# Kernel tuning notes

Measured on AMD Instinct MI355X. Metric: run time of the kernel, lower is better.

Reference implementation:

```python
import jax, jax.numpy as jnp
import numpy as np

N = 100000      # nodes (patches)
NNZ = 800000    # incidence (node, hyperedge) pairs from H.coo()
E = 16384       # hyperedges
IN = 128        # in_dim == hidden_dim (residual path active)
HID = 128
HEADS = 4
HD = HID // HEADS   # 32, per-head out_dim
QD = 64             # type_query_dim
L = 2               # n_layers
NT = 4              # n_node_types
ET = 3              # n_edge_types


def setup_inputs() -> dict:
    key = jax.random.key(0)
    ks = jax.random.split(key, 12)
    f32 = jnp.float32
    return {
        "x": jax.random.normal(ks[0], (N, IN), f32),
        "node_types": jax.random.randint(ks[1], (N,), 0, NT, jnp.int32),
        "node_idx": jax.random.randint(ks[2], (NNZ,), 0, N, jnp.int32),
        "edge_idx": jax.random.randint(ks[3], (NNZ,), 0, E, jnp.int32),
        "edge_type": jax.random.randint(ks[4], (E,), 0, ET, jnp.int32),
        # per-layer, per-head parameters (leading axes L, HEADS)
        "type_query": (jax.random.normal(ks[5], (L, HEADS, NT, QD), f32) * 0.02),
        "fc1_w": jax.random.normal(ks[6], (L, HEADS, IN + QD, 32), f32) / np.sqrt(IN + QD),
        "fc1_b": jnp.zeros((L, HEADS, 32), f32),
        "fc2_w": jax.random.normal(ks[7], (L, HEADS, 32, 1), f32) / np.sqrt(32.0),
        "fc2_b": jnp.zeros((L, HEADS, 1), f32),
        "Wq": jax.random.normal(ks[8], (L, HEADS, IN, HD), f32) / np.sqrt(IN),
        "Wv": jax.random.normal(ks[9], (L, HEADS, IN, HD), f32) / np.sqrt(IN),
        "edge_ctx": jax.random.normal(ks[10], (L, HEADS, ET, HD), f32) * 0.02,
        "ln_g": jnp.ones((L, HID), f32),
        "ln_b": jnp.zeros((L, HID), f32),
    }


def _seg_softmax(a, seg, num):
    # scatter_softmax over segments `seg` (stable: subtract per-segment max)
    m = jax.ops.segment_max(a, seg, num_segments=num)
    ex = jnp.exp(a - m[seg])
    s = jax.ops.segment_sum(ex, seg, num_segments=num)
    return ex / s[seg]


def _head(h, node_types, node_idx, edge_idx, edge_type, tq, w1, b1, w2, b2, wq, wv, ec):
    # CascadedHyperGAT.forward, one head
    sig = tq[node_types]                                      # (N, QD)
    z = jnp.tanh(jnp.concatenate([h, sig], axis=1) @ w1 + b1)  # (N, 32)
    alpha_type = jax.nn.sigmoid(z @ w2 + b2)[:, 0]             # (N,)
    Q = h @ wq                                                 # (N, HD)
    V = h @ wv                                                 # (N, HD)
    ctx = ec[edge_type][edge_idx]                              # (NNZ, HD)
    a = jnp.sum(Q[node_idx] * ctx, axis=1)                     # (NNZ,)
    a = jnp.where(a >= 0, a, 0.2 * a)                          # leaky_relu(0.2)
    a = a * alpha_type[node_idx]
    attn = _seg_softmax(a, edge_idx, E)                        # (NNZ,)
    edge_feat = jax.ops.segment_sum(attn[:, None] * V[node_idx], edge_idx, num_segments=E)
    node_feat = jax.ops.segment_sum(attn[:, None] * edge_feat[edge_idx], node_idx, num_segments=N)
    return node_feat, edge_feat


def _layernorm(h, g, b, eps=1e-5):
    mu = h.mean(-1, keepdims=True)
    var = ((h - mu) ** 2).mean(-1, keepdims=True)
    return (h - mu) * jax.lax.rsqrt(var + eps) * g + b


def reference(x, node_types, node_idx, edge_idx, edge_type,
              type_query, fc1_w, fc1_b, fc2_w, fc2_b, Wq, Wv, edge_ctx, ln_g, ln_b):
    head_v = jax.vmap(_head, in_axes=(None, None, None, None, None, 0, 0, 0, 0, 0, 0, 0, 0))
    stats = [x]
    h = x
    for l in range(L):  # small static layer count
        nf, _ = head_v(h, node_types, node_idx, edge_idx, edge_type,
                       type_query[l], fc1_w[l], fc1_b[l], fc2_w[l], fc2_b[l],
                       Wq[l], Wv[l], edge_ctx[l])            # (HEADS, N, HD)
        hn = jnp.transpose(nf, (1, 0, 2)).reshape(h.shape[0], -1)  # concat heads -> (N, HID)
        if hn.shape == h.shape:
            hn = hn + h                                       # residual (dims match)
        h = _layernorm(hn, ln_g[l], ln_b[l])
        stats.append(h)
    return jnp.concatenate(stats, axis=-1)                    # (N, IN + HID*L)
```

## Files before the change

kernel.cpp:

```cpp
#include <hip/hip_runtime.h>
#include <math.h>

#define HEADS 4
#define HD 32
#define QD 64
#define DIN 128
#define NTYPES 4
#define ETYPES 3
#define CAP 512
#define WTC 272

typedef __attribute__((ext_vector_type(8))) short bf16x8;
typedef __attribute__((ext_vector_type(4))) float f32x4;
typedef unsigned short ushort_t;

static inline int cdiv(int a, int b){ return (a + b - 1) / b; }

__device__ inline unsigned short f2bf(float f){
  unsigned u = __float_as_uint(f);
  unsigned r = (u + 0x7FFF + ((u >> 16) & 1)) >> 16;
  return (unsigned short)r;
}
__device__ inline float bf2f(unsigned short u){ return __uint_as_float(((unsigned)u) << 16); }

__device__ inline float lgt_get(const ushort_t* __restrict__ lgt, int n, int et, int hh){
  uint2 lg = *(const uint2*)((const char*)lgt + (size_t)n*24 + et*8);
  unsigned u = (hh & 2) ? lg.y : lg.x;
  return bf2f((hh & 1) ? (ushort_t)(u >> 16) : (ushort_t)(u & 0xffff));
}

__device__ inline void accum8(float* ef, uint4 w, float e){
  ef[0] += e*bf2f((ushort_t)(w.x & 0xffff)); ef[1] += e*bf2f((ushort_t)(w.x >> 16));
  ef[2] += e*bf2f((ushort_t)(w.y & 0xffff)); ef[3] += e*bf2f((ushort_t)(w.y >> 16));
  ef[4] += e*bf2f((ushort_t)(w.z & 0xffff)); ef[5] += e*bf2f((ushort_t)(w.z >> 16));
  ef[6] += e*bf2f((ushort_t)(w.w & 0xffff)); ef[7] += e*bf2f((ushort_t)(w.w >> 16));
}


__global__ __launch_bounds__(256) void hist_k(const int* __restrict__ node_idx,
                                              const int* __restrict__ edge_idx,
                                              int* __restrict__ cnt,
                                              uint2* __restrict__ ranks, int E, int NNZ)
{
  int i = blockIdx.x*256 + threadIdx.x;
  if (i < NNZ){
    unsigned re = (unsigned)atomicAdd(&cnt[edge_idx[i]], 1);
    unsigned rn = (unsigned)atomicAdd(&cnt[E + node_idx[i]], 1);
    uint2 r; r.x = re; r.y = rn;
    ranks[i] = r;
  }
}

__global__ __launch_bounds__(1024) void scan_pass1(const int* __restrict__ in, int* __restrict__ bsums, int n)
{
  __shared__ int sd[1024];
  int i = blockIdx.x*1024 + threadIdx.x;
  sd[threadIdx.x] = (i < n) ? in[i] : 0;
  __syncthreads();
  for (int s = 512; s > 0; s >>= 1){
    if (threadIdx.x < s) sd[threadIdx.x] += sd[threadIdx.x + s];
    __syncthreads();
  }
  if (threadIdx.x == 0) bsums[blockIdx.x] = sd[0];
}

__global__ __launch_bounds__(1024) void scan_pass2(int* __restrict__ bsums, int nb)
{
  __shared__ int sd[1024];
  int v = (threadIdx.x < nb) ? bsums[threadIdx.x] : 0;
  sd[threadIdx.x] = v;
  __syncthreads();
  for (int s = 1; s < 1024; s <<= 1){
    int t = (threadIdx.x >= s) ? sd[threadIdx.x - s] : 0;
    __syncthreads();
    sd[threadIdx.x] += t;
    __syncthreads();
  }
  if (threadIdx.x < nb) bsums[threadIdx.x] = sd[threadIdx.x] - v;
}

__global__ __launch_bounds__(1024) void scan_pass3(const int* __restrict__ in, const int* __restrict__ bsums,
                                                   int* __restrict__ out, int n)
{
  __shared__ int sd[1024];
  int i = blockIdx.x*1024 + threadIdx.x;
  int v = (i < n) ? in[i] : 0;
  sd[threadIdx.x] = v;
  __syncthreads();
  for (int s = 1; s < 1024; s <<= 1){
    int t = (threadIdx.x >= s) ? sd[threadIdx.x - s] : 0;
    __syncthreads();
    sd[threadIdx.x] += t;
    __syncthreads();
  }
  if (i < n) out[i] = bsums[blockIdx.x] + sd[threadIdx.x] - v;
}

__global__ __launch_bounds__(256) void scatter_k(const int* __restrict__ node_idx, const int* __restrict__ edge_idx,
                                                 const uint2* __restrict__ ranks,
                                                 const int* __restrict__ off,
                                                 uint2* __restrict__ srtE_rec, int E, int NNZ)
{
  int i = blockIdx.x*256 + threadIdx.x;
  if (i >= NNZ) return;
  int n = node_idx[i], e = edge_idx[i];
  uint2 r = ranks[i];
  int pe = off[e] + (int)r.x;
  int pn = off[E + n] - NNZ + (int)r.y;
  uint2 rec; rec.x = (unsigned)n; rec.y = (unsigned)pn;
  srtE_rec[pe] = rec;
}


__global__ __launch_bounds__(128) void wtprep_k(const float* __restrict__ w1, const float* __restrict__ wv,
                                                short* __restrict__ Wt, int L)
{
  int c = blockIdx.x % 256, l = blockIdx.x / 256;
  int k = threadIdx.x;
  int hh = (c >> 5) & 3, j = c & 31;
  float v;
  if (c < 128) v = w1[((((size_t)l*HEADS + hh)*(DIN+QD)) + k)*32 + j];
  else         v = wv[((((size_t)l*HEADS + hh)*DIN) + k)*32 + j];
  Wt[((size_t)l*WTC + c)*128 + k] = (short)f2bf(v);
}

__global__ __launch_bounds__(128) void wqc_k(const float* __restrict__ wq, const float* __restrict__ ec,
                                             short* __restrict__ Wt)
{
  int b = blockIdx.x;
  int l = b / 12, c = b % 12, h = c / 3, et = c % 3;
  int k = threadIdx.x;
  const float* wrow = wq + ((((size_t)l*HEADS + h)*DIN) + k)*32;
  const float* ecp  = ec + (((size_t)l*HEADS + h)*ETYPES + et)*32;
  float s = 0.f;
  #pragma unroll
  for (int d = 0; d < 32; d++) s += wrow[d] * ecp[d];
  Wt[((size_t)l*WTC + 256 + c)*128 + k] = (short)f2bf(s);
}

__global__ __launch_bounds__(32) void sbias_k(const float* __restrict__ tq, const float* __restrict__ w1,
                                              const float* __restrict__ b1, float* __restrict__ sbias)
{
  int b = blockIdx.x;
  int ty = b % NTYPES; int hh = (b / NTYPES) % HEADS; int l = b / (NTYPES*HEADS);
  int j = threadIdx.x;
  const float* tqp = tq + (((size_t)l*HEADS + hh)*NTYPES + ty)*QD;
  const float* w1p = w1 + ((size_t)l*HEADS + hh)*(DIN+QD)*32;
  float s = b1[((size_t)l*HEADS + hh)*32 + j];
  for (int k = 0; k < QD; k++) s += tqp[k] * w1p[(size_t)(DIN + k)*32 + j];
  sbias[(size_t)b*32 + j] = s;
}


__device__ inline void load_afrag(const float* __restrict__ h, int hstride, int N,
                                  int rbase, int mf, int l15, int l4, int kk, bf16x8& a)
{
  int row = rbase + mf*16 + l15;
  int rr = (row < N) ? row : (N-1);
  const float* pa = h + (size_t)rr*hstride + kk*32 + l4*8;
  float4 f0 = *(const float4*)pa;
  float4 f1 = *(const float4*)(pa + 4);
  a[0] = (short)f2bf(f0.x); a[1] = (short)f2bf(f0.y);
  a[2] = (short)f2bf(f0.z); a[3] = (short)f2bf(f0.w);
  a[4] = (short)f2bf(f1.x); a[5] = (short)f2bf(f1.y);
  a[6] = (short)f2bf(f1.z); a[7] = (short)f2bf(f1.w);
}


__global__ __launch_bounds__(256) void gemma_k(
    const float* __restrict__ h, int hstride,
    const short* __restrict__ Wt,
    const int* __restrict__ node_types,
    const float* __restrict__ sbias,
    const float* __restrict__ w2,
    const float* __restrict__ b2,
    ushort_t* __restrict__ lgt,
    int N)
{
  __shared__ float alds[128][HEADS];
  int lane = threadIdx.x & 63, wvid = threadIdx.x >> 6;
  int wr = wvid >> 1, wc = wvid & 1;
  int l15 = lane & 15, l4 = lane >> 4;
  int rbase = blockIdx.x*128 + wr*64;

  f32x4 acc[4][4] = {};
  f32x4 acc_e[4] = {};

  #pragma unroll
  for (int kk = 0; kk < 4; kk++){
    bf16x8 a[4], b[4];
    #pragma unroll
    for (int mf = 0; mf < 4; mf++) load_afrag(h, hstride, N, rbase, mf, l15, l4, kk, a[mf]);
    #pragma unroll
    for (int cf = 0; cf < 4; cf++){
      int col = wc*64 + cf*16 + l15;
      b[cf] = *(const bf16x8*)(Wt + (size_t)col*128 + kk*32 + l4*8);
    }
    #pragma unroll
    for (int mf = 0; mf < 4; mf++)
      #pragma unroll
      for (int cf = 0; cf < 4; cf++)
        acc[mf][cf] = __builtin_amdgcn_mfma_f32_16x16x32_bf16(a[mf], b[cf], acc[mf][cf], 0, 0, 0);
    if (wc == 0){
      int ecol = 256 + ((l15 < 12) ? l15 : 11);
      bf16x8 be = *(const bf16x8*)(Wt + (size_t)ecol*128 + kk*32 + l4*8);
      #pragma unroll
      for (int mf = 0; mf < 4; mf++)
        acc_e[mf] = __builtin_amdgcn_mfma_f32_16x16x32_bf16(a[mf], be, acc_e[mf], 0, 0, 0);
    }
  }

  #pragma unroll
  for (int mf = 0; mf < 4; mf++){
    int rw[4], ty[4];
    #pragma unroll
    for (int r = 0; r < 4; r++){
      rw[r] = rbase + mf*16 + l4*4 + r;
      ty[r] = (rw[r] < N) ? node_types[rw[r]] : 0;
    }
    #pragma unroll
    for (int p = 0; p < 2; p++){
      int hh = wc*2 + p;
      float w2a = w2[hh*32 + l15];
      float w2b = w2[hh*32 + 16 + l15];
      float b2v = b2[hh];
      #pragma unroll
      for (int r = 0; r < 4; r++){
        const float* sb = sbias + ((size_t)hh*NTYPES + ty[r])*32;
        float z0 = acc[mf][2*p  ][r] + sb[l15];
        float z1 = acc[mf][2*p+1][r] + sb[16 + l15];
        float t0 = 1.f - 2.f/(__expf(2.f*z0) + 1.f);
        float t1 = 1.f - 2.f/(__expf(2.f*z1) + 1.f);
        float val = t0*w2a + t1*w2b;
        val += __shfl_xor(val, 1); val += __shfl_xor(val, 2);
        val += __shfl_xor(val, 4); val += __shfl_xor(val, 8);
        if (l15 == 0)
          alds[wr*64 + mf*16 + l4*4 + r][hh] = 1.f/(1.f + __expf(-(val + b2v)));
      }
    }
  }
  __syncthreads();

  if (wc == 0 && l15 < 12){
    int hq = l15 / 3, et = l15 % 3;
    #pragma unroll
    for (int mf = 0; mf < 4; mf++){
      #pragma unroll
      for (int r = 0; r < 4; r++){
        int rowloc = wr*64 + mf*16 + l4*4 + r;
        int row = blockIdx.x*128 + rowloc;
        if (row < N){
          float s = acc_e[mf][r] * alds[rowloc][hq];
          s = (s >= 0.f) ? s : 0.2f*s;
          lgt[(size_t)row*12 + et*4 + hq] = f2bf(s);
        }
      }
    }
  }
}


__global__ __launch_bounds__(256) void gemmv_k(
    const float* __restrict__ h, int hstride,
    const short* __restrict__ Wt,
    ushort_t* __restrict__ vb,
    int N)
{
  int lane = threadIdx.x & 63, wvid = threadIdx.x >> 6;
  int wr = wvid >> 1, wc = wvid & 1;
  int l15 = lane & 15, l4 = lane >> 4;
  int rbase = blockIdx.x*128 + wr*64;

  f32x4 acc[4][4] = {};

  #pragma unroll
  for (int kk = 0; kk < 4; kk++){
    bf16x8 a[4], b[4];
    #pragma unroll
    for (int mf = 0; mf < 4; mf++) load_afrag(h, hstride, N, rbase, mf, l15, l4, kk, a[mf]);
    #pragma unroll
    for (int cf = 0; cf < 4; cf++){
      int col = 128 + wc*64 + cf*16 + l15;
      b[cf] = *(const bf16x8*)(Wt + (size_t)col*128 + kk*32 + l4*8);
    }
    #pragma unroll
    for (int mf = 0; mf < 4; mf++)
      #pragma unroll
      for (int cf = 0; cf < 4; cf++)
        acc[mf][cf] = __builtin_amdgcn_mfma_f32_16x16x32_bf16(a[mf], b[cf], acc[mf][cf], 0, 0, 0);
  }

  #pragma unroll
  for (int mf = 0; mf < 4; mf++){
    #pragma unroll
    for (int r = 0; r < 4; r++){
      int row = rbase + mf*16 + l4*4 + r;
      if (row < N){
        #pragma unroll
        for (int cf = 0; cf < 4; cf++){
          int c = wc*64 + cf*16 + l15;
          int hh = c >> 5, d = c & 31;
          vb[((size_t)hh*N + row)*32 + d] = f2bf(acc[mf][cf][r]);
        }
      }
    }
  }
}


__global__ __launch_bounds__(256) void k2b_f(
    const ushort_t* __restrict__ lgt, const ushort_t* __restrict__ vb,
    const uint2* __restrict__ srtE_rec, const int* __restrict__ edge_off, const int* __restrict__ cnt_e,
    const int* __restrict__ edge_type,
    ushort_t* __restrict__ efb,
    uint4* __restrict__ attn_rec,
    int N, int E)
{
  __shared__ float lbuf[HEADS][CAP];
  __shared__ int   nbuf[CAP];
  __shared__ int   pnbuf[CAP];
  __shared__ float mi[HEADS][2];

  int e = blockIdx.x;
  int off = edge_off[e], cnt = cnt_e[e];
  if (cnt == 0) return;
  int lane = threadIdx.x & 63, hh = threadIdx.x >> 6;
  int et = edge_type[e];

  if (cnt <= CAP){
    for (int j = threadIdx.x; j < cnt; j += 256){
      uint2 rc = srtE_rec[off + j];
      uint2 lg = *(const uint2*)((const char*)lgt + (size_t)rc.x*24 + et*8);
      lbuf[0][j] = bf2f((ushort_t)(lg.x & 0xffff));
      lbuf[1][j] = bf2f((ushort_t)(lg.x >> 16));
      lbuf[2][j] = bf2f((ushort_t)(lg.y & 0xffff));
      lbuf[3][j] = bf2f((ushort_t)(lg.y >> 16));
      nbuf[j] = (int)rc.x;
      pnbuf[j] = (int)rc.y;
    }
    __syncthreads();

    float mloc = -INFINITY;
    for (int j = lane; j < cnt; j += 64) mloc = fmaxf(mloc, lbuf[hh][j]);
    #pragma unroll
    for (int sh = 32; sh > 0; sh >>= 1) mloc = fmaxf(mloc, __shfl_xor(mloc, sh));
    float m = mloc;

    int g4 = lane & 3, grp16 = lane >> 2;
    float ef[8] = {0.f,0.f,0.f,0.f,0.f,0.f,0.f,0.f};
    float ssum = 0.f;
    const int cm1 = cnt - 1;
    const ushort_t* vbh = vb + (size_t)hh*N*32;
    for (int jj = 0; jj < cnt; jj += 64){
      int j0 = jj + grp16, j1 = j0 + 16, j2 = j0 + 32, j3 = j0 + 48;
      int n0 = nbuf[(j0 < cm1) ? j0 : cm1];
      int n1 = nbuf[(j1 < cm1) ? j1 : cm1];
      int n2 = nbuf[(j2 < cm1) ? j2 : cm1];
      int n3 = nbuf[(j3 < cm1) ? j3 : cm1];
      uint4 w0 = *(const uint4*)&vbh[(size_t)n0*32 + 8*g4];
      uint4 w1 = *(const uint4*)&vbh[(size_t)n1*32 + 8*g4];
      uint4 w2 = *(const uint4*)&vbh[(size_t)n2*32 + 8*g4];
      uint4 w3 = *(const uint4*)&vbh[(size_t)n3*32 + 8*g4];
      float e0 = (j0 < cnt) ? __expf(lbuf[hh][j0] - m) : 0.f;
      float e1 = (j1 < cnt) ? __expf(lbuf[hh][j1] - m) : 0.f;
      float e2 = (j2 < cnt) ? __expf(lbuf[hh][j2] - m) : 0.f;
      float e3 = (j3 < cnt) ? __expf(lbuf[hh][j3] - m) : 0.f;
      accum8(ef, w0, e0);
      accum8(ef, w1, e1);
      accum8(ef, w2, e2);
      accum8(ef, w3, e3);
      ssum += e0 + e1 + e2 + e3;
    }
    #pragma unroll
    for (int sh = 4; sh <= 32; sh <<= 1){
      #pragma unroll
      for (int q = 0; q < 8; q++) ef[q] += __shfl_xor(ef[q], sh);
      ssum += __shfl_xor(ssum, sh);
    }
    float inv = 1.0f / ssum;
    if (grp16 == 0){
      uint4 o;
      o.x = (unsigned)f2bf(ef[0]*inv) | ((unsigned)f2bf(ef[1]*inv) << 16);
      o.y = (unsigned)f2bf(ef[2]*inv) | ((unsigned)f2bf(ef[3]*inv) << 16);
      o.z = (unsigned)f2bf(ef[4]*inv) | ((unsigned)f2bf(ef[5]*inv) << 16);
      o.w = (unsigned)f2bf(ef[6]*inv) | ((unsigned)f2bf(ef[7]*inv) << 16);
      *(uint4*)&efb[(size_t)e*128 + hh*32 + 8*g4] = o;
    }
    if (lane == 0){ mi[hh][0] = m; mi[hh][1] = inv; }
    __syncthreads();

    if (hh == 0){
      for (int j = lane; j < cnt; j += 64){
        int pn = pnbuf[j];
        float a0 = __expf(lbuf[0][j] - mi[0][0]) * mi[0][1];
        float a1 = __expf(lbuf[1][j] - mi[1][0]) * mi[1][1];
        float a2 = __expf(lbuf[2][j] - mi[2][0]) * mi[2][1];
        float a3 = __expf(lbuf[3][j] - mi[3][0]) * mi[3][1];
        uint4 o;
        o.x = (unsigned)e;
        o.y = (unsigned)f2bf(a0) | ((unsigned)f2bf(a1) << 16);
        o.z = (unsigned)f2bf(a2) | ((unsigned)f2bf(a3) << 16);
        o.w = 0u;
        attn_rec[pn] = o;
      }
    }
  } else {
    int g = lane & 15, grp = lane >> 4;
    float mloc = -INFINITY;
    for (int j = lane; j < cnt; j += 64)
      mloc = fmaxf(mloc, lgt_get(lgt, (int)srtE_rec[off + j].x, et, hh));
    #pragma unroll
    for (int sh = 32; sh > 0; sh >>= 1) mloc = fmaxf(mloc, __shfl_xor(mloc, sh));
    float m = mloc;

    float ef0 = 0.f, ef1 = 0.f, ssum = 0.f;
    for (int jj = 0; jj < cnt; jj += 4){
      int j = jj + grp;
      if (j < cnt){
        int n = (int)srtE_rec[off + j].x;
        float ex = __expf(lgt_get(lgt, n, et, hh) - m);
        unsigned vw = *(const unsigned*)&vb[((size_t)hh*N + n)*32 + 2*g];
        ef0 += ex * bf2f((unsigned short)(vw & 0xffff));
        ef1 += ex * bf2f((unsigned short)(vw >> 16));
        ssum += ex;
      }
    }
    ef0 += __shfl_xor(ef0, 16); ef0 += __shfl_xor(ef0, 32);
    ef1 += __shfl_xor(ef1, 16); ef1 += __shfl_xor(ef1, 32);
    ssum += __shfl_xor(ssum, 16); ssum += __shfl_xor(ssum, 32);
    float inv = 1.0f / ssum;
    if (grp == 0){
      unsigned w = (unsigned)f2bf(ef0*inv) | ((unsigned)f2bf(ef1*inv) << 16);
      *(unsigned*)&efb[(size_t)e*128 + hh*32 + 2*g] = w;
    }
    for (int j = lane; j < cnt; j += 64){
      uint2 rc = srtE_rec[off + j];
      float ex = __expf(lgt_get(lgt, (int)rc.x, et, hh) - m);
      ushort_t* p = (ushort_t*)&attn_rec[rc.y];
      p[2 + hh] = f2bf(ex * inv);
      if (hh == 0){
        ((unsigned*)p)[0] = (unsigned)e;
        ((unsigned*)p)[3] = 0u;
      }
    }
  }
}


__global__ __launch_bounds__(256) void k2c(
    const uint4* __restrict__ attn_rec,
    const int* __restrict__ node_off, const int* __restrict__ cnt_n, int noff_shift,
    const ushort_t* __restrict__ efb,
    const float* __restrict__ h_in, int hstride,
    const float* __restrict__ ln_g, const float* __restrict__ ln_b,
    float* __restrict__ out, int out_stride, int out_col, int do_xcopy, int N, int E)
{
  int wv = threadIdx.x >> 6, lane = threadIdx.x & 63;
  int n = blockIdx.x*4 + wv;
  if (n >= N) return;
  int off = node_off[n] - noff_shift, cnt = cnt_n[n];
  int hh = lane >> 4;
  float nf0 = 0.f, nf1 = 0.f;

  for (int j0 = 0; j0 < cnt; j0 += 8){
    int mm = cnt - j0; if (mm > 8) mm = 8;
    uint4 rc = make_uint4(0u, 0u, 0u, 0u);
    if (lane < mm) rc = attn_rec[off + j0 + lane];
    unsigned w[8]; float av[8];
    #pragma unroll
    for (int j = 0; j < 8; j++){
      unsigned ej = (unsigned)__shfl((int)rc.x, j);
      unsigned ay = (unsigned)__shfl((int)rc.y, j);
      unsigned az = (unsigned)__shfl((int)rc.z, j);
      unsigned u = (hh & 2) ? az : ay;
      float a = bf2f((hh & 1) ? (ushort_t)(u >> 16) : (ushort_t)(u & 0xffff));
      av[j] = (j < mm) ? a : 0.f;
      w[j] = *(const unsigned*)&efb[(size_t)ej*128 + 2*lane];
    }
    #pragma unroll
    for (int j = 0; j < 8; j++){
      nf0 += av[j] * bf2f((ushort_t)(w[j] & 0xffff));
      nf1 += av[j] * bf2f((ushort_t)(w[j] >> 16));
    }
  }

  float2 hr = *(const float2*)&h_in[(size_t)n*hstride + 2*lane];
  if (do_xcopy)
    *(float2*)&out[(size_t)n*out_stride + 2*lane] = hr;
  float hn0 = nf0 + hr.x, hn1 = nf1 + hr.y;

  float s = hn0 + hn1;
  #pragma unroll
  for (int sh = 32; sh > 0; sh >>= 1) s += __shfl_xor(s, sh);
  float mu = s * (1.0f/128.0f);
  float d0 = hn0 - mu, d1 = hn1 - mu;
  float s2 = d0*d0 + d1*d1;
  #pragma unroll
  for (int sh = 32; sh > 0; sh >>= 1) s2 += __shfl_xor(s2, sh);
  float r = rsqrtf(s2*(1.0f/128.0f) + 1e-5f);

  float2 g2 = *(const float2*)&ln_g[2*lane];
  float2 b2 = *(const float2*)&ln_b[2*lane];
  float2 o2;
  o2.x = d0*r*g2.x + b2.x;
  o2.y = d1*r*g2.y + b2.y;
  *(float2*)&out[(size_t)n*out_stride + out_col + 2*lane] = o2;
}


extern "C" void kernel_launch(void* const* d_in, const int* in_sizes, int n_in,
                              void* d_out, int out_size, void* d_ws, size_t ws_size,
                              hipStream_t stream)
{
  const float* x          = (const float*)d_in[0];
  const int*   node_types = (const int*)  d_in[1];
  const int*   node_idx   = (const int*)  d_in[2];
  const int*   edge_idx   = (const int*)  d_in[3];
  const int*   edge_type  = (const int*)  d_in[4];
  const float* type_query = (const float*)d_in[5];
  const float* fc1_w      = (const float*)d_in[6];
  const float* fc1_b      = (const float*)d_in[7];
  const float* fc2_w      = (const float*)d_in[8];
  const float* fc2_b      = (const float*)d_in[9];
  const float* Wq         = (const float*)d_in[10];
  const float* Wv         = (const float*)d_in[11];
  const float* edge_ctx   = (const float*)d_in[12];
  const float* ln_g       = (const float*)d_in[13];
  const float* ln_b       = (const float*)d_in[14];

  const int N   = in_sizes[1];
  const int NNZ = in_sizes[2];
  const int E   = in_sizes[4];
  const int L   = 2;
  const int EN  = E + N;

  char* ws = (char*)d_ws;
  size_t o = 0;
  auto alloc = [&](size_t bytes)->void*{
    void* p = ws + o;
    o = (o + bytes + 255) & ~(size_t)255;
    return p;
  };
  int* cnt       = (int*)alloc((size_t)EN*4);
  int* off       = (int*)alloc((size_t)(EN+1)*4);
  uint2* ranks   = (uint2*)alloc((size_t)NNZ*8);
  uint2* srtE_rec= (uint2*)alloc((size_t)NNZ*8);
  int* bsum      = (int*)alloc((size_t)1024*4);
  uint4* attn_rec = (uint4*)alloc((size_t)NNZ*16);
  ushort_t* vb      = (ushort_t*)alloc((size_t)HEADS*N*32*2);
  ushort_t* lgt     = (ushort_t*)alloc((size_t)N*12*2);
  ushort_t* efb     = (ushort_t*)alloc((size_t)E*128*2);
  short*    Wt      = (short*)alloc((size_t)L*WTC*128*2);
  float*    sbias   = (float*)alloc((size_t)L*HEADS*NTYPES*32*4);
  if (o > ws_size) return;

  hipMemsetAsync(cnt, 0, (size_t)EN*4, stream);

  hist_k<<<cdiv(NNZ,256),256,0,stream>>>(node_idx, edge_idx, cnt, ranks, E, NNZ);

  int nb = cdiv(EN,1024);
  scan_pass1<<<nb,1024,0,stream>>>(cnt, bsum, EN);
  scan_pass2<<<1,1024,0,stream>>>(bsum, nb);
  scan_pass3<<<nb,1024,0,stream>>>(cnt, bsum, off, EN);

  scatter_k<<<cdiv(NNZ,256),256,0,stream>>>(node_idx, edge_idx, ranks, off, srtE_rec, E, NNZ);

  wtprep_k<<<L*256,128,0,stream>>>(fc1_w, Wv, Wt, L);
  wqc_k<<<L*12,128,0,stream>>>(Wq, edge_ctx, Wt);
  sbias_k<<<L*HEADS*NTYPES,32,0,stream>>>(type_query, fc1_w, fc1_b, sbias);

  for (int l = 0; l < L; l++){
    const float* hin = (l == 0) ? x : ((const float*)d_out + 128);
    int hstride = (l == 0) ? DIN : (3*DIN);

    gemma_k<<<cdiv(N,128),256,0,stream>>>(
        hin, hstride,
        Wt + (size_t)l*WTC*128,
        node_types,
        sbias + (size_t)l*HEADS*NTYPES*32,
        fc2_w + (size_t)l*HEADS*32,
        fc2_b + (size_t)l*HEADS,
        lgt, N);

    gemmv_k<<<cdiv(N,128),256,0,stream>>>(
        hin, hstride,
        Wt + (size_t)l*WTC*128,
        vb, N);

    k2b_f<<<E,256,0,stream>>>(lgt, vb, srtE_rec, off, cnt,
                              edge_type, efb, attn_rec, N, E);

    k2c<<<cdiv(N,4),256,0,stream>>>(attn_rec, off + E, cnt + E, NNZ, efb,
                                    hin, hstride,
                                    ln_g + (size_t)l*DIN, ln_b + (size_t)l*DIN,
                                    (float*)d_out, 3*DIN, DIN + l*DIN, (l == 0) ? 1 : 0, N, E);
  }
}
```

Baseline: 526.8 us.

## Fuse attention-logit and value GEMMs into one kernel with LDS-staged input

```diff
diff --git a/kernel.cpp b/kernel.cpp
--- a/kernel.cpp
+++ b/kernel.cpp
@@ -152,22 +152,7 @@
 }
 
 
-__device__ inline void load_afrag(const float* __restrict__ h, int hstride, int N,
-                                  int rbase, int mf, int l15, int l4, int kk, bf16x8& a)
-{
-  int row = rbase + mf*16 + l15;
-  int rr = (row < N) ? row : (N-1);
-  const float* pa = h + (size_t)rr*hstride + kk*32 + l4*8;
-  float4 f0 = *(const float4*)pa;
-  float4 f1 = *(const float4*)(pa + 4);
-  a[0] = (short)f2bf(f0.x); a[1] = (short)f2bf(f0.y);
-  a[2] = (short)f2bf(f0.z); a[3] = (short)f2bf(f0.w);
-  a[4] = (short)f2bf(f1.x); a[5] = (short)f2bf(f1.y);
-  a[6] = (short)f2bf(f1.z); a[7] = (short)f2bf(f1.w);
-}
-
-
-__global__ __launch_bounds__(256) void gemma_k(
+__global__ __launch_bounds__(512) void gemm_f3(
     const float* __restrict__ h, int hstride,
     const short* __restrict__ Wt,
     const int* __restrict__ node_types,
@@ -175,25 +160,42 @@
     const float* __restrict__ w2,
     const float* __restrict__ b2,
     ushort_t* __restrict__ lgt,
+    ushort_t* __restrict__ vb,
     int N)
 {
+  __shared__ ushort_t hlds[128][136];
   __shared__ float alds[128][HEADS];
-  int lane = threadIdx.x & 63, wvid = threadIdx.x >> 6;
-  int wr = wvid >> 1, wc = wvid & 1;
+  int t = threadIdx.x;
+  int lane = t & 63, wvid = t >> 6;
+  int wr = wvid >> 2, wc = wvid & 3;
   int l15 = lane & 15, l4 = lane >> 4;
-  int rbase = blockIdx.x*128 + wr*64;
+  int rbase0 = blockIdx.x*128;
+  int rbase = rbase0 + wr*64;
+
+  #pragma unroll
+  for (int it = 0; it < 8; it++){
+    int idx = it*512 + t;
+    int r = idx >> 5, c4 = (idx & 31)*4;
+    int rr = rbase0 + r; rr = (rr < N) ? rr : (N-1);
+    float4 f = *(const float4*)(h + (size_t)rr*hstride + c4);
+    ushort_t* p = &hlds[r][c4];
+    p[0] = f2bf(f.x); p[1] = f2bf(f.y); p[2] = f2bf(f.z); p[3] = f2bf(f.w);
+  }
+  __syncthreads();
 
   f32x4 acc[4][4] = {};
   f32x4 acc_e[4] = {};
+  int colbase = (wc < 2) ? wc*64 : (128 + (wc - 2)*64);
 
   #pragma unroll
   for (int kk = 0; kk < 4; kk++){
     bf16x8 a[4], b[4];
     #pragma unroll
-    for (int mf = 0; mf < 4; mf++) load_afrag(h, hstride, N, rbase, mf, l15, l4, kk, a[mf]);
+    for (int mf = 0; mf < 4; mf++)
+      a[mf] = *(const bf16x8*)&hlds[wr*64 + mf*16 + l15][kk*32 + l4*8];
     #pragma unroll
     for (int cf = 0; cf < 4; cf++){
-      int col = wc*64 + cf*16 + l15;
+      int col = colbase + cf*16 + l15;
       b[cf] = *(const bf16x8*)(Wt + (size_t)col*128 + kk*32 + l4*8);
     }
     #pragma unroll
@@ -210,32 +212,50 @@
     }
   }
 
-  #pragma unroll
-  for (int mf = 0; mf < 4; mf++){
-    int rw[4], ty[4];
-    #pragma unroll
-    for (int r = 0; r < 4; r++){
-      rw[r] = rbase + mf*16 + l4*4 + r;
-      ty[r] = (rw[r] < N) ? node_types[rw[r]] : 0;
-    }
-    #pragma unroll
-    for (int p = 0; p < 2; p++){
-      int hh = wc*2 + p;
-      float w2a = w2[hh*32 + l15];
-      float w2b = w2[hh*32 + 16 + l15];
-      float b2v = b2[hh];
+  if (wc < 2){
+    #pragma unroll
+    for (int mf = 0; mf < 4; mf++){
+      int rw[4], ty[4];
       #pragma unroll
       for (int r = 0; r < 4; r++){
-        const float* sb = sbias + ((size_t)hh*NTYPES + ty[r])*32;
-        float z0 = acc[mf][2*p  ][r] + sb[l15];
-        float z1 = acc[mf][2*p+1][r] + sb[16 + l15];
-        float t0 = 1.f - 2.f/(__expf(2.f*z0) + 1.f);
-        float t1 = 1.f - 2.f/(__expf(2.f*z1) + 1.f);
-        float val = t0*w2a + t1*w2b;
-        val += __shfl_xor(val, 1); val += __shfl_xor(val, 2);
-        val += __shfl_xor(val, 4); val += __shfl_xor(val, 8);
-        if (l15 == 0)
-          alds[wr*64 + mf*16 + l4*4 + r][hh] = 1.f/(1.f + __expf(-(val + b2v)));
+        rw[r] = rbase + mf*16 + l4*4 + r;
+        ty[r] = (rw[r] < N) ? node_types[rw[r]] : 0;
+      }
+      #pragma unroll
+      for (int p = 0; p < 2; p++){
+        int hh = wc*2 + p;
+        float w2a = w2[hh*32 + l15];
+        float w2b = w2[hh*32 + 16 + l15];
+        float b2v = b2[hh];
+        #pragma unroll
+        for (int r = 0; r < 4; r++){
+          const float* sb = sbias + ((size_t)hh*NTYPES + ty[r])*32;
+          float z0 = acc[mf][2*p  ][r] + sb[l15];
+          float z1 = acc[mf][2*p+1][r] + sb[16 + l15];
+          float t0 = 1.f - 2.f/(__expf(2.f*z0) + 1.f);
+          float t1 = 1.f - 2.f/(__expf(2.f*z1) + 1.f);
+          float val = t0*w2a + t1*w2b;
+          val += __shfl_xor(val, 1); val += __shfl_xor(val, 2);
+          val += __shfl_xor(val, 4); val += __shfl_xor(val, 8);
+          if (l15 == 0)
+            alds[wr*64 + mf*16 + l4*4 + r][hh] = 1.f/(1.f + __expf(-(val + b2v)));
+        }
+      }
+    }
+  } else {
+    #pragma unroll
+    for (int mf = 0; mf < 4; mf++){
+      #pragma unroll
+      for (int r = 0; r < 4; r++){
+        int row = rbase + mf*16 + l4*4 + r;
+        if (row < N){
+          #pragma unroll
+          for (int cf = 0; cf < 4; cf++){
+            int c = (wc - 2)*64 + cf*16 + l15;
+            int hh = c >> 5, d = c & 31;
+            vb[((size_t)hh*N + row)*32 + d] = f2bf(acc[mf][cf][r]);
+          }
+        }
       }
     }
   }
@@ -248,59 +268,11 @@
       #pragma unroll
       for (int r = 0; r < 4; r++){
         int rowloc = wr*64 + mf*16 + l4*4 + r;
-        int row = blockIdx.x*128 + rowloc;
+        int row = rbase0 + rowloc;
         if (row < N){
           float s = acc_e[mf][r] * alds[rowloc][hq];
           s = (s >= 0.f) ? s : 0.2f*s;
           lgt[(size_t)row*12 + et*4 + hq] = f2bf(s);
-        }
-      }
-    }
-  }
-}
-
-
-__global__ __launch_bounds__(256) void gemmv_k(
-    const float* __restrict__ h, int hstride,
-    const short* __restrict__ Wt,
-    ushort_t* __restrict__ vb,
-    int N)
-{
-  int lane = threadIdx.x & 63, wvid = threadIdx.x >> 6;
-  int wr = wvid >> 1, wc = wvid & 1;
-  int l15 = lane & 15, l4 = lane >> 4;
-  int rbase = blockIdx.x*128 + wr*64;
-
-  f32x4 acc[4][4] = {};
-
-  #pragma unroll
-  for (int kk = 0; kk < 4; kk++){
-    bf16x8 a[4], b[4];
-    #pragma unroll
-    for (int mf = 0; mf < 4; mf++) load_afrag(h, hstride, N, rbase, mf, l15, l4, kk, a[mf]);
-    #pragma unroll
-    for (int cf = 0; cf < 4; cf++){
-      int col = 128 + wc*64 + cf*16 + l15;
-      b[cf] = *(const bf16x8*)(Wt + (size_t)col*128 + kk*32 + l4*8);
-    }
-    #pragma unroll
-    for (int mf = 0; mf < 4; mf++)
-      #pragma unroll
-      for (int cf = 0; cf < 4; cf++)
-        acc[mf][cf] = __builtin_amdgcn_mfma_f32_16x16x32_bf16(a[mf], b[cf], acc[mf][cf], 0, 0, 0);
-  }
-
-  #pragma unroll
-  for (int mf = 0; mf < 4; mf++){
-    #pragma unroll
-    for (int r = 0; r < 4; r++){
-      int row = rbase + mf*16 + l4*4 + r;
-      if (row < N){
-        #pragma unroll
-        for (int cf = 0; cf < 4; cf++){
-          int c = wc*64 + cf*16 + l15;
-          int hh = c >> 5, d = c & 31;
-          vb[((size_t)hh*N + row)*32 + d] = f2bf(acc[mf][cf][r]);
         }
       }
     }
@@ -573,19 +545,14 @@
     const float* hin = (l == 0) ? x : ((const float*)d_out + 128);
     int hstride = (l == 0) ? DIN : (3*DIN);
 
-    gemma_k<<<cdiv(N,128),256,0,stream>>>(
+    gemm_f3<<<cdiv(N,128),512,0,stream>>>(
         hin, hstride,
         Wt + (size_t)l*WTC*128,
         node_types,
         sbias + (size_t)l*HEADS*NTYPES*32,
         fc2_w + (size_t)l*HEADS*32,
         fc2_b + (size_t)l*HEADS,
-        lgt, N);
-
-    gemmv_k<<<cdiv(N,128),256,0,stream>>>(
-        hin, hstride,
-        Wt + (size_t)l*WTC*128,
-        vb, N);
+        lgt, vb, N);
 
     k2b_f<<<E,256,0,stream>>>(lgt, vb, srtE_rec, off, cnt,
                               edge_type, efb, attn_rec, N, E);
```

Result: no change. 534.5 us (+1.5%).
